# Kernel tuning notes

Measured on AMD Instinct MI355X. Metric: run time of the kernel, lower is better.

## Reference

```python
import jax, jax.numpy as jnp
import numpy as np

TOPK, ALPHA, BETA, EPS = 13, 1.0, 6.0, 1e-9


def setup_inputs() -> dict:
    key = jax.random.key(0)
    k0, k1, k2, k3, k4, k5 = jax.random.split(key, 6)
    bs, C, A = 64, 80, 8400
    pd_scores = jax.random.uniform(k0, (bs, C, A), dtype=jnp.float32)
    # predicted boxes in x1y1x2y2 (normalized coords), guaranteed x2>x1, y2>y1
    xy1 = jax.random.uniform(k1, (bs, 2, A), dtype=jnp.float32) * 0.6
    wh = jax.random.uniform(k2, (bs, 2, A), dtype=jnp.float32) * 0.4 + 0.01
    pd_bboxes = jnp.concatenate([xy1, xy1 + wh], axis=1)  # (bs,4,A)
    gxy1 = jax.random.uniform(k3, (bs, 2), dtype=jnp.float32) * 0.6
    gwh = jax.random.uniform(k4, (bs, 2), dtype=jnp.float32) * 0.4 + 0.01
    gt_bboxes = jnp.concatenate([gxy1, gxy1 + gwh], axis=1)  # (bs,4)
    gt_labels = jax.random.randint(k5, (64,), 0, C)
    return {"pd_scores": pd_scores, "pd_bboxes": pd_bboxes,
            "gt_labels": gt_labels, "gt_bboxes": gt_bboxes}


def reference(pd_scores, pd_bboxes, gt_labels, gt_bboxes):
    bs, _, num_anchors = pd_scores.shape
    # ---- IoU: gt (bs,4,1) vs pred (bs,4,A) -> (bs,A)
    b1 = gt_bboxes[:, :, None]                       # (bs,4,1)
    px1y1, px2y2 = b1[:, 0:2], b1[:, 2:4]            # (bs,2,1)
    gx1y1, gx2y2 = pd_bboxes[:, 0:2], pd_bboxes[:, 2:4]  # (bs,2,A)
    overlap = jnp.clip(jnp.minimum(px2y2, gx2y2) - jnp.maximum(px1y1, gx1y1), 0).prod(axis=-2)  # (bs,A)
    area1 = jnp.clip(px2y2 - px1y1, 0).prod(axis=-2)  # (bs,1)
    area2 = jnp.clip(gx2y2 - gx1y1, 0).prod(axis=-2)  # (bs,A)
    overlaps = overlap / (area1 + area2 - overlap + EPS)  # (bs,A)
    # ---- alignment metric
    bbox_scores = pd_scores[jnp.arange(bs), gt_labels]  # (bs,A) gather per-image class row
    align_metric = (bbox_scores ** ALPHA) * (overlaps ** BETA)
    # ---- top-k candidate mask (scatter instead of one_hot+sum)
    topk_metrics, topk_idxs = jax.lax.top_k(align_metric, TOPK)   # (bs,TOPK)
    topk_mask = topk_metrics.max(axis=-1, keepdims=True) > EPS    # (bs,1)
    topk_idxs = jnp.where(topk_mask, topk_idxs, 0)
    cnt = jnp.zeros((bs, num_anchors), jnp.int32).at[
        jnp.arange(bs)[:, None], topk_idxs].add(1)
    mask_pos = jnp.where(cnt > 1, 0, cnt).astype(align_metric.dtype)  # (bs,A)
    # ---- normalized target scores (faithful to original reduction axes)
    am = align_metric * mask_pos
    pos_align_metrics = am.max(axis=-1, keepdims=True)            # (bs,1)
    pos_overlaps = (overlaps * mask_pos).max(axis=-1, keepdims=True)  # (bs,1)
    norm_align_metric = (am * pos_overlaps / (pos_align_metrics + EPS)).max(axis=-2)[:, None]  # (A,1)
    target_scores = gt_labels.astype(norm_align_metric.dtype) * norm_align_metric  # (A,bs)
    return target_scores, mask_pos
```

## Files before the change

kernel.cpp:

```cpp
#include <hip/hip_runtime.h>
#include <hip/hip_bf16.h>

#define NA 8400
#define BS 64
#define NC 80
#define TOPK 13
#define EPSF 1e-9f

__global__ __launch_bounds__(256) void assign_kernel(
    const float* __restrict__ pd_scores,
    const float* __restrict__ pd_bboxes,
    const int*   __restrict__ gt_labels,
    const float* __restrict__ gt_bboxes,
    float*       __restrict__ out_mask,
    float*       __restrict__ norm)
{
    __shared__ float s_align[NA];
    __shared__ float s_redv[4];
    __shared__ int   s_redi[4];
    __shared__ int   s_sel[TOPK];
    __shared__ float s_selv[TOPK];
    __shared__ float s_selov[TOPK];
    __shared__ float s_mask;

    const int b = blockIdx.x;
    const int t = threadIdx.x;
    const int wave = t >> 6, lane = t & 63;

    const float p1x = gt_bboxes[b * 4 + 0];
    const float p1y = gt_bboxes[b * 4 + 1];
    const float p2x = gt_bboxes[b * 4 + 2];
    const float p2y = gt_bboxes[b * 4 + 3];
    const float area1 = fmaxf(p2x - p1x, 0.f) * fmaxf(p2y - p1y, 0.f);
    const int lbl = gt_labels[b];
    const float* sc = pd_scores + (size_t)b * NC * NA + (size_t)lbl * NA;
    const float* bb = pd_bboxes + (size_t)b * 4 * NA;

    for (int a = t; a < NA; a += 256) {
        float g1x = bb[0 * NA + a];
        float g1y = bb[1 * NA + a];
        float g2x = bb[2 * NA + a];
        float g2y = bb[3 * NA + a];
        float wx = fmaxf(fminf(p2x, g2x) - fmaxf(p1x, g1x), 0.f);
        float wy = fmaxf(fminf(p2y, g2y) - fmaxf(p1y, g1y), 0.f);
        float ovl = wx * wy;
        float area2 = fmaxf(g2x - g1x, 0.f) * fmaxf(g2y - g1y, 0.f);
        float o = ovl / (area1 + area2 - ovl + EPSF);
        float o2 = o * o;
        float score = sc[a];
        s_align[a] = score * (o2 * o2 * o2);
    }
    __syncthreads();

    for (int j = 0; j < TOPK; ++j) {
        float bv = -2.f;
        int   bi = 0x7fffffff;
        for (int a = t; a < NA; a += 256) {
            float v = s_align[a];
            if (v > bv) { bv = v; bi = a; }
        }
        #pragma unroll
        for (int off = 32; off > 0; off >>= 1) {
            float ov_ = __shfl_down(bv, off);
            int   oi_ = __shfl_down(bi, off);
            if (ov_ > bv || (ov_ == bv && oi_ < bi)) { bv = ov_; bi = oi_; }
        }
        if (lane == 0) { s_redv[wave] = bv; s_redi[wave] = bi; }
        __syncthreads();
        if (t == 0) {
            for (int w = 1; w < 4; ++w) {
                float ov_ = s_redv[w]; int oi_ = s_redi[w];
                if (ov_ > bv || (ov_ == bv && oi_ < bi)) { bv = ov_; bi = oi_; }
            }
            s_sel[j] = bi; s_selv[j] = bv;
            s_align[bi] = -1.0f;
        }
        __syncthreads();
    }

    if (t < TOPK) {
        int a = s_sel[t];
        float g1x = bb[0 * NA + a];
        float g1y = bb[1 * NA + a];
        float g2x = bb[2 * NA + a];
        float g2y = bb[3 * NA + a];
        float wx = fmaxf(fminf(p2x, g2x) - fmaxf(p1x, g1x), 0.f);
        float wy = fmaxf(fminf(p2y, g2y) - fmaxf(p1y, g1y), 0.f);
        float ovl = wx * wy;
        float area2 = fmaxf(g2x - g1x, 0.f) * fmaxf(g2y - g1y, 0.f);
        s_selov[t] = ovl / (area1 + area2 - ovl + EPSF);
    }
    __syncthreads();

    if (t == 0) {
        float pos_align = s_selv[0];
        bool mask = pos_align > EPSF;
        s_mask = mask ? 1.f : 0.f;
        if (mask) {
            float pos_ov = 0.f;
            for (int j = 0; j < TOPK; ++j) pos_ov = fmaxf(pos_ov, s_selov[j]);
            for (int j = 0; j < TOPK; ++j) {
                float v = (s_selv[j] * pos_ov) / (pos_align + EPSF);
                atomicMax((int*)&norm[s_sel[j]], __float_as_int(v));
            }
        }
    }
    __syncthreads();

    const float maskf = s_mask;
    for (int a = t; a < NA; a += 256) {
        bool sel = (s_align[a] == -1.0f) && (maskf > 0.5f);
        out_mask[(size_t)b * NA + a] = sel ? 1.0f : 0.0f;
    }
}

__global__ __launch_bounds__(256) void scores_kernel(
    const float* __restrict__ norm,
    const int*   __restrict__ gt_labels,
    float*       __restrict__ out0)
{
    int idx = blockIdx.x * 256 + threadIdx.x;
    if (idx >= NA * BS) return;
    int b = idx & (BS - 1);
    int a = idx >> 6;
    float v = (float)gt_labels[b] * norm[a];
    out0[idx] = v;
}

extern "C" void kernel_launch(void* const* d_in, const int* in_sizes, int n_in,
                              void* d_out, int out_size, void* d_ws, size_t ws_size,
                              hipStream_t stream) {
    const float* pd_scores = (const float*)d_in[0];
    const float* pd_bboxes = (const float*)d_in[1];
    const int*   gt_labels = (const int*)d_in[2];
    const float* gt_bboxes = (const float*)d_in[3];

    float* out0     = (float*)d_out;
    float* out_mask = out0 + (size_t)NA * BS;
    float* norm     = (float*)d_ws;

    hipMemsetAsync(norm, 0, NA * sizeof(float), stream);
    assign_kernel<<<BS, 256, 0, stream>>>(pd_scores, pd_bboxes, gt_labels,
                                          gt_bboxes, out_mask, norm);
    scores_kernel<<<(NA * BS + 255) / 256, 256, 0, stream>>>(norm, gt_labels, out0);
}
```

Measured before the change: 239.1 us.

## Replace block-wide iterative top-k with per-wave register top-k and merge

Each wave now owns a contiguous segment of 2100 anchors, holding the alignment values and IoUs in registers. It finds a local top-13 using only wave shuffles, with no block barriers. A single wave then merges the 52 candidates, computes the normalisation, and issues the atomics. The mask is written by comparing each anchor against the 13 winners. This removes the 26 block-wide syncs and the repeated shared-memory scans, and reuses the IoUs instead of recomputing them. In exchange it uses heavy register arrays (66 floats per thread) and a fully unrolled selection loop.

```diff
diff --git a/kernel.cpp b/kernel.cpp
--- a/kernel.cpp
+++ b/kernel.cpp
@@ -6,6 +6,8 @@
 #define NC 80
 #define TOPK 13
 #define EPSF 1e-9f
+#define SEG 2100
+#define KMAX 33
 
 __global__ __launch_bounds__(256) void assign_kernel(
     const float* __restrict__ pd_scores,
@@ -15,17 +17,17 @@
     float*       __restrict__ out_mask,
     float*       __restrict__ norm)
 {
-    __shared__ float s_align[NA];
-    __shared__ float s_redv[4];
-    __shared__ int   s_redi[4];
-    __shared__ int   s_sel[TOPK];
-    __shared__ float s_selv[TOPK];
-    __shared__ float s_selov[TOPK];
+    __shared__ float s_cv[4 * TOPK];
+    __shared__ int   s_ci[4 * TOPK];
+    __shared__ float s_cov[4 * TOPK];
+    __shared__ int   s_win[TOPK];
     __shared__ float s_mask;
 
     const int b = blockIdx.x;
     const int t = threadIdx.x;
     const int wave = t >> 6, lane = t & 63;
+    const int seg_lo = wave * SEG;
+    const int seg_hi = seg_lo + SEG;
 
     const float p1x = gt_bboxes[b * 4 + 0];
     const float p1y = gt_bboxes[b * 4 + 1];
@@ -36,81 +38,105 @@
     const float* sc = pd_scores + (size_t)b * NC * NA + (size_t)lbl * NA;
     const float* bb = pd_bboxes + (size_t)b * 4 * NA;
 
-    for (int a = t; a < NA; a += 256) {
-        float g1x = bb[0 * NA + a];
-        float g1y = bb[1 * NA + a];
-        float g2x = bb[2 * NA + a];
-        float g2y = bb[3 * NA + a];
+    float lv[KMAX], lov[KMAX];
+    #pragma unroll
+    for (int k = 0; k < KMAX; ++k) {
+        int a = seg_lo + lane + (k << 6);
+        bool ok = a < seg_hi;
+        int aa = ok ? a : seg_lo;
+        float g1x = bb[0 * NA + aa];
+        float g1y = bb[1 * NA + aa];
+        float g2x = bb[2 * NA + aa];
+        float g2y = bb[3 * NA + aa];
         float wx = fmaxf(fminf(p2x, g2x) - fmaxf(p1x, g1x), 0.f);
         float wy = fmaxf(fminf(p2y, g2y) - fmaxf(p1y, g1y), 0.f);
         float ovl = wx * wy;
         float area2 = fmaxf(g2x - g1x, 0.f) * fmaxf(g2y - g1y, 0.f);
         float o = ovl / (area1 + area2 - ovl + EPSF);
         float o2 = o * o;
-        float score = sc[a];
-        s_align[a] = score * (o2 * o2 * o2);
+        float score = sc[aa];
+        lv[k]  = ok ? score * (o2 * o2 * o2) : -1.0f;
+        lov[k] = o;
+    }
+
+    unsigned long long selmask = 0ULL;
+    float cand_v = -2.f; int cand_i = 0x7fffffff; float cand_ov = 0.f;
+    for (int j = 0; j < TOPK; ++j) {
+        float mv = -2.f; int mk = 0; float mov = 0.f;
+        #pragma unroll
+        for (int k = 0; k < KMAX; ++k) {
+            bool excl = (selmask >> k) & 1ULL;
+            float v = excl ? -2.f : lv[k];
+            if (v > mv) { mv = v; mk = k; mov = lov[k]; }
+        }
+        int mi = seg_lo + lane + (mk << 6);
+        float bv = mv; int bi = mi; float bov = mov;
+        #pragma unroll
+        for (int off = 1; off < 64; off <<= 1) {
+            float ov_ = __shfl_xor(bv, off);
+            int   oi_ = __shfl_xor(bi, off);
+            float oo_ = __shfl_xor(bov, off);
+            if (ov_ > bv || (ov_ == bv && oi_ < bi)) { bv = ov_; bi = oi_; bov = oo_; }
+        }
+        if (mi == bi) selmask |= 1ULL << mk;
+        if (lane == j) { cand_v = bv; cand_i = bi; cand_ov = bov; }
+    }
+    if (lane < TOPK) {
+        s_cv [wave * TOPK + lane] = cand_v;
+        s_ci [wave * TOPK + lane] = cand_i;
+        s_cov[wave * TOPK + lane] = cand_ov;
     }
     __syncthreads();
 
-    for (int j = 0; j < TOPK; ++j) {
-        float bv = -2.f;
-        int   bi = 0x7fffffff;
-        for (int a = t; a < NA; a += 256) {
-            float v = s_align[a];
-            if (v > bv) { bv = v; bi = a; }
+    if (wave == 0) {
+        const int NC4 = 4 * TOPK;
+        float v  = lane < NC4 ? s_cv[lane]  : -2.f;
+        int   ci = lane < NC4 ? s_ci[lane]  : 0x7fffffff;
+        float ov = lane < NC4 ? s_cov[lane] : 0.f;
+        float pos_align = 0.f, pos_ov = 0.f;
+        float wv_sel = 0.f; int wi_sel = 0;
+        for (int j = 0; j < TOPK; ++j) {
+            float bv = v; int bi = ci; float bov = ov;
+            #pragma unroll
+            for (int off = 1; off < 64; off <<= 1) {
+                float ov_ = __shfl_xor(bv, off);
+                int   oi_ = __shfl_xor(bi, off);
+                float oo_ = __shfl_xor(bov, off);
+                if (ov_ > bv || (ov_ == bv && oi_ < bi)) { bv = ov_; bi = oi_; bov = oo_; }
+            }
+            if (j == 0) pos_align = bv;
+            pos_ov = fmaxf(pos_ov, bov);
+            if (lane == j) { wv_sel = bv; wi_sel = bi; }
+            if (ci == bi) v = -2.f;
         }
-        #pragma unroll
-        for (int off = 32; off > 0; off >>= 1) {
-            float ov_ = __shfl_down(bv, off);
-            int   oi_ = __shfl_down(bi, off);
-            if (ov_ > bv || (ov_ == bv && oi_ < bi)) { bv = ov_; bi = oi_; }
-        }
-        if (lane == 0) { s_redv[wave] = bv; s_redi[wave] = bi; }
-        __syncthreads();
-        if (t == 0) {
-            for (int w = 1; w < 4; ++w) {
-                float ov_ = s_redv[w]; int oi_ = s_redi[w];
-                if (ov_ > bv || (ov_ == bv && oi_ < bi)) { bv = ov_; bi = oi_; }
-            }
-            s_sel[j] = bi; s_selv[j] = bv;
-            s_align[bi] = -1.0f;
-        }
-        __syncthreads();
-    }
-
-    if (t < TOPK) {
-        int a = s_sel[t];
-        float g1x = bb[0 * NA + a];
-        float g1y = bb[1 * NA + a];
-        float g2x = bb[2 * NA + a];
-        float g2y = bb[3 * NA + a];
-        float wx = fmaxf(fminf(p2x, g2x) - fmaxf(p1x, g1x), 0.f);
-        float wy = fmaxf(fminf(p2y, g2y) - fmaxf(p1y, g1y), 0.f);
-        float ovl = wx * wy;
-        float area2 = fmaxf(g2x - g1x, 0.f) * fmaxf(g2y - g1y, 0.f);
-        s_selov[t] = ovl / (area1 + area2 - ovl + EPSF);
-    }
-    __syncthreads();
-
-    if (t == 0) {
-        float pos_align = s_selv[0];
-        bool mask = pos_align > EPSF;
-        s_mask = mask ? 1.f : 0.f;
-        if (mask) {
-            float pos_ov = 0.f;
-            for (int j = 0; j < TOPK; ++j) pos_ov = fmaxf(pos_ov, s_selov[j]);
-            for (int j = 0; j < TOPK; ++j) {
-                float v = (s_selv[j] * pos_ov) / (pos_align + EPSF);
-                atomicMax((int*)&norm[s_sel[j]], __float_as_int(v));
+        float mask = pos_align > EPSF ? 1.f : 0.f;
+        if (lane == 0) s_mask = mask;
+        if (lane < TOPK) {
+            s_win[lane] = wi_sel;
+            if (mask != 0.f) {
+                float vv = (wv_sel * pos_ov) / (pos_align + EPSF);
+                atomicMax((int*)&norm[wi_sel], __float_as_int(vv));
             }
         }
     }
     __syncthreads();
 
     const float maskf = s_mask;
-    for (int a = t; a < NA; a += 256) {
-        bool sel = (s_align[a] == -1.0f) && (maskf > 0.5f);
-        out_mask[(size_t)b * NA + a] = sel ? 1.0f : 0.0f;
+    int w0  = s_win[0],  w1  = s_win[1],  w2  = s_win[2],  w3 = s_win[3];
+    int w4  = s_win[4],  w5  = s_win[5],  w6  = s_win[6],  w7 = s_win[7];
+    int w8  = s_win[8],  w9  = s_win[9],  w10 = s_win[10], w11 = s_win[11];
+    int w12 = s_win[12];
+    float* om = out_mask + (size_t)b * NA;
+    #pragma unroll
+    for (int k = 0; k < KMAX; ++k) {
+        int a = seg_lo + lane + (k << 6);
+        if (a < seg_hi) {
+            bool sel = (a == w0) | (a == w1) | (a == w2) | (a == w3) |
+                       (a == w4) | (a == w5) | (a == w6) | (a == w7) |
+                       (a == w8) | (a == w9) | (a == w10) | (a == w11) |
+                       (a == w12);
+            om[a] = (sel && maskf > 0.5f) ? 1.0f : 0.0f;
+        }
     }
 }
 
@@ -123,8 +149,7 @@
     if (idx >= NA * BS) return;
     int b = idx & (BS - 1);
     int a = idx >> 6;
-    float v = (float)gt_labels[b] * norm[a];
-    out0[idx] = v;
+    out0[idx] = (float)gt_labels[b] * norm[a];
 }
 
 extern "C" void kernel_launch(void* const* d_in, const int* in_sizes, int n_in,
```

Result: slower. 265.5 us (+11.0%).
